# Performance work log

Hardware: AMD Instinct MI355X
Metric: run time of the kernel (lower is better)

The kernel has to match this reference:

```python
import jax, jax.numpy as jnp
import numpy as np

B, S, E = 4, 4096, 512
DK, DV = 64, 64


def setup_inputs() -> dict:
    key = jax.random.key(0)
    ks = jax.random.split(key, 7)
    s_e = 1.0 / np.sqrt(E)
    return {
        "embedding_matrix": jax.random.normal(ks[0], (B, S, E), dtype=jnp.float32),
        # torch Linear init ~ U(-1/sqrt(in), 1/sqrt(in)); stored here as [in, out]
        "Wq_w": jax.random.uniform(ks[1], (E, DK), jnp.float32, -s_e, s_e),
        "Wq_b": jax.random.uniform(ks[2], (DK,), jnp.float32, -s_e, s_e),
        "Wk_w": jax.random.uniform(ks[3], (E, DK), jnp.float32, -s_e, s_e),
        "Wk_b": jax.random.uniform(ks[4], (DK,), jnp.float32, -s_e, s_e),
        "Wv_w": jax.random.uniform(ks[5], (E, DV), jnp.float32, -s_e, s_e),
        "Wv_b": jax.random.uniform(ks[6], (DV,), jnp.float32, -s_e, s_e),
    }


def reference(embedding_matrix, Wq_w, Wq_b, Wk_w, Wk_b, Wv_w, Wv_b):
    # Single-head causal attention, faithful to the torch module (mask=True).
    Q = embedding_matrix @ Wq_w + Wq_b            # [B, S, DK]
    K = embedding_matrix @ Wk_w + Wk_b            # [B, S, DK]
    V = embedding_matrix @ Wv_w + Wv_b            # [B, S, DV]
    dk = K.shape[-1]
    scores = jnp.einsum('bqd,bkd->bqk', Q, K) / jnp.sqrt(jnp.asarray(dk, Q.dtype))
    seq_len = scores.shape[-1]
    causal = jnp.tril(jnp.ones((seq_len, seq_len), dtype=bool))  # keep lower-tri
    scores = jnp.where(causal[None, :, :], scores, -jnp.inf)
    attn = jax.nn.softmax(scores.astype(jnp.float32), axis=-1)
    return jnp.einsum('bqk,bkd->bqd', attn, V)
```

## Files before the change

kernel.cpp:

```cpp
#include <hip/hip_runtime.h>
#include <hip/hip_bf16.h>

#define B_ 4
#define S_ 4096
#define E_ 512
#define D_ 64

typedef float  f32x4  __attribute__((ext_vector_type(4)));
typedef float  f32x16 __attribute__((ext_vector_type(16)));
typedef short  s16x8  __attribute__((ext_vector_type(8)));

__device__ inline short f2bf(float f){
  unsigned u = __builtin_bit_cast(unsigned, f);
  u += 0x7fffu + ((u >> 16) & 1u);
  return (short)(u >> 16);
}
__device__ inline unsigned bfpack(float a, float b){
  unsigned ua = __builtin_bit_cast(unsigned, a);
  unsigned ub = __builtin_bit_cast(unsigned, b);
  ua += 0x7fffu + ((ua >> 16) & 1u);
  ub += 0x7fffu + ((ub >> 16) & 1u);
  return (ua >> 16) | (ub & 0xffff0000u);
}
__device__ inline float ex2(float x){ return __builtin_amdgcn_exp2f(x); }

#define QSCALE 0.18033688f


__global__ __launch_bounds__(256) void prep_kernel(const float* __restrict__ Wq,
                                                   const float* __restrict__ Wk,
                                                   const float* __restrict__ Wv,
                                                   short* __restrict__ Wtf){
  int o = blockIdx.x * 256 + threadIdx.x;
  int cbi = o >> 13;
  int l   = (o >> 3) & 63;
  int j   = o & 7;
  int kk  = (o >> 9) & 15;
  int n = cbi * 16 + (l & 15);
  int k = kk * 32 + (l >> 4) * 8 + j;
  const float* W = (n < 64) ? Wq : (n < 128 ? Wk : Wv);
  float v = W[k * 64 + (n & 63)];
  if (n < 64) v *= QSCALE;
  Wtf[o] = f2bf(v);
}

__global__ __launch_bounds__(256) void proj_kernel(const float* __restrict__ X,
                                                   const short* __restrict__ Wtf,
                                                   const float* __restrict__ bq,
                                                   const float* __restrict__ bk,
                                                   const float* __restrict__ bv,
                                                   short* __restrict__ Qf,
                                                   short* __restrict__ Kf,
                                                   short* __restrict__ Vf){
  __shared__ short Xs[1024 * 8];
  __shared__ short Os[16][136];
  __shared__ short OsT[64][24];

  const int tid = threadIdx.x;
  const int l = tid & 63, w = tid >> 6;
  const int c = l & 15,  g = l >> 4;
  const int r0 = blockIdx.x * 16;
  const int t  = (r0 >> 5) & 127;
  const int h  = (r0 >> 4) & 1;
  const int b  = r0 >> 12;

#pragma unroll
  for (int i = 0; i < 4; i++){
    int ch  = i * 256 + tid;
    int row = ch >> 6, gr = ch & 63;
    const float* xp = X + (size_t)(r0 + row) * E_ + gr * 8;
    f32x4 a0 = *reinterpret_cast<const f32x4*>(xp);
    f32x4 a1 = *reinterpret_cast<const f32x4*>(xp + 4);
    s16x8 hv;
#pragma unroll
    for (int q = 0; q < 4; q++){ hv[q] = f2bf(a0[q]); hv[4+q] = f2bf(a1[q]); }
    *reinterpret_cast<s16x8*>(&Xs[(row * 64 + (gr ^ (row & 7))) * 8]) = hv;
  }
  __syncthreads();

  f32x4 acc[3];
#pragma unroll
  for (int j = 0; j < 3; j++) acc[j] = (f32x4){0.f,0.f,0.f,0.f};

  for (int kk = 0; kk < 16; kk++){
    s16x8 af = *reinterpret_cast<const s16x8*>(&Xs[(c * 64 + ((kk * 4 + g) ^ (c & 7))) * 8]);
#pragma unroll
    for (int j = 0; j < 3; j++){
      int cbi = w * 3 + j;
      s16x8 bf = *reinterpret_cast<const s16x8*>(Wtf + (((size_t)(cbi * 16 + kk)) << 9) + (l << 3));
      acc[j] = __builtin_amdgcn_mfma_f32_16x16x32_bf16(af, bf, acc[j], 0, 0, 0);
    }
  }

#pragma unroll
  for (int j = 0; j < 3; j++){
    int cbi = w * 3 + j;
    int d = ((cbi & 3) << 4) + c;
    if (cbi < 8){
      float bias = (cbi < 4) ? bq[d] * QSCALE : bk[d];
      int col = (cbi < 4) ? d : (64 + d);
#pragma unroll
      for (int r = 0; r < 4; r++) Os[g * 4 + r][col] = f2bf(acc[j][r] + bias);
    } else {
      float bias = bv[d];
      union { unsigned long long u; short s[4]; } pk;
#pragma unroll
      for (int r = 0; r < 4; r++) pk.s[r] = f2bf(acc[j][r] + bias);
      *reinterpret_cast<unsigned long long*>(&OsT[d][g * 4]) = pk.u;
    }
  }
  __syncthreads();

  const size_t tbase = ((size_t)(b * 128 + t)) << 11;
  {
    int q = tid & 127;
    int N = q >> 5, hd = (q >> 4) & 1, lo16 = q & 15;
    int d0 = N * 16 + hd * 8;
    int col = (tid < 128) ? d0 : (64 + d0);
    s16x8 vv = *reinterpret_cast<const s16x8*>(&Os[lo16][col]);
    short* dst = (tid < 128 ? Qf : Kf) + tbase + N * 512 + hd * 256 + (h * 16 + lo16) * 8;
    *reinterpret_cast<s16x8*>(dst) = vv;
  }
  if (tid < 128){
    int hf = tid >> 6, ht = (tid >> 5) & 1, dl = tid & 31;
    s16x8 vv = *reinterpret_cast<const s16x8*>(&OsT[hf * 32 + dl][ht * 8]);
    short* dst = Vf + tbase + (h + 2 * hf) * 512 + ht * 256 + dl * 8;
    *reinterpret_cast<s16x8*>(dst) = vv;
  }
}

__global__ __launch_bounds__(512, 4) void attn_kernel(const short* __restrict__ Qf,
                                                      const short* __restrict__ Kf,
                                                      const short* __restrict__ Vf,
                                                      float* __restrict__ out){
  __shared__ float accw[8][32][64];
  __shared__ float mlw[8][32][2];
  __shared__ float corrw[8][32];

  const int tid = threadIdx.x;
  const int w  = tid >> 6;
  const int l  = tid & 63;
  const int lo = l & 31, hi = l >> 5;
  const int bid = blockIdx.x;
  const int b  = bid >> 7;
  const int t  = 127 - (bid & 127);
  const int q0 = t << 5;

  const short* qb = Qf + (((size_t)(b * 128 + t)) << 11) + (l << 3);
  s16x8 qf0 = *reinterpret_cast<const s16x8*>(qb);
  s16x8 qf1 = *reinterpret_cast<const s16x8*>(qb + 512);
  s16x8 qf2 = *reinterpret_cast<const s16x8*>(qb + 1024);
  s16x8 qf3 = *reinterpret_cast<const s16x8*>(qb + 1536);

  float m = -1e30f, ls = 0.f;
  f32x16 acc0, acc1;
#pragma unroll
  for (int r = 0; r < 16; r++){ acc0[r] = 0.f; acc1[r] = 0.f; }

  const int nkt = t + 1;
  for (int kt = w; kt < nkt; kt += 8){
    const int k0 = kt << 5;
    const short* kb = Kf + (((size_t)(b * 128 + kt)) << 11) + (l << 3);
    s16x8 kf0 = *reinterpret_cast<const s16x8*>(kb);
    s16x8 kf1 = *reinterpret_cast<const s16x8*>(kb + 512);
    s16x8 kf2 = *reinterpret_cast<const s16x8*>(kb + 1024);
    s16x8 kf3 = *reinterpret_cast<const s16x8*>(kb + 1536);
    const short* vb = Vf + (((size_t)(b * 128 + kt)) << 11) + (l << 3);
    s16x8 v00 = *reinterpret_cast<const s16x8*>(vb);
    s16x8 v01 = *reinterpret_cast<const s16x8*>(vb + 512);
    s16x8 v10 = *reinterpret_cast<const s16x8*>(vb + 1024);
    s16x8 v11 = *reinterpret_cast<const s16x8*>(vb + 1536);

    f32x16 s;
#pragma unroll
    for (int r = 0; r < 16; r++) s[r] = 0.f;
    s = __builtin_amdgcn_mfma_f32_32x32x16_bf16(kf0, qf0, s, 0, 0, 0);
    s = __builtin_amdgcn_mfma_f32_32x32x16_bf16(kf1, qf1, s, 0, 0, 0);
    s = __builtin_amdgcn_mfma_f32_32x32x16_bf16(kf2, qf2, s, 0, 0, 0);
    s = __builtin_amdgcn_mfma_f32_32x32x16_bf16(kf3, qf3, s, 0, 0, 0);

    if (k0 == q0){
#pragma unroll
      for (int r = 0; r < 16; r++){
        int key = (r & 3) + ((r >> 2) << 3) + (hi << 2);
        if (key > lo) s[r] = -1e30f;
      }
    }

    float x0 = fmaxf(s[0], s[1]),  x1 = fmaxf(s[2], s[3]);
    float x2 = fmaxf(s[4], s[5]),  x3 = fmaxf(s[6], s[7]);
    float x4 = fmaxf(s[8], s[9]),  x5 = fmaxf(s[10], s[11]);
    float x6 = fmaxf(s[12], s[13]), x7 = fmaxf(s[14], s[15]);
    float pm = fmaxf(fmaxf(fmaxf(x0, x1), fmaxf(x2, x3)),
                     fmaxf(fmaxf(x4, x5), fmaxf(x6, x7)));
    pm = fmaxf(pm, __shfl_xor(pm, 32));

    if (!__all(pm - m <= 8.0f)){
      float mn = fmaxf(m, pm);
      float corr = ex2(m - mn);
      if (hi == 0) corrw[w][lo] = corr;
      asm volatile("s_waitcnt lgkmcnt(0)" ::: "memory");
      __builtin_amdgcn_sched_barrier(0);
      f32x4 c0 = *reinterpret_cast<const f32x4*>(&corrw[w][(hi << 2)]);
      f32x4 c1 = *reinterpret_cast<const f32x4*>(&corrw[w][8 + (hi << 2)]);
      f32x4 c2 = *reinterpret_cast<const f32x4*>(&corrw[w][16 + (hi << 2)]);
      f32x4 c3 = *reinterpret_cast<const f32x4*>(&corrw[w][24 + (hi << 2)]);
#pragma unroll
      for (int r = 0; r < 4; r++){
        acc0[r]      *= c0[r]; acc1[r]      *= c0[r];
        acc0[4 + r]  *= c1[r]; acc1[4 + r]  *= c1[r];
        acc0[8 + r]  *= c2[r]; acc1[8 + r]  *= c2[r];
        acc0[12 + r] *= c3[r]; acc1[12 + r] *= c3[r];
      }
      ls *= corr;
      m = mn;
    }

#pragma unroll
    for (int r = 0; r < 16; r++) s[r] = ex2(s[r] - m);

    float y0 = s[0]+s[1], y1 = s[2]+s[3], y2 = s[4]+s[5], y3 = s[6]+s[7];
    float y4 = s[8]+s[9], y5 = s[10]+s[11], y6 = s[12]+s[13], y7 = s[14]+s[15];
    float rs = ((y0+y1)+(y2+y3)) + ((y4+y5)+(y6+y7));
    rs += __shfl_xor(rs, 32);
    ls += rs;

    unsigned pk0 = bfpack(s[0], s[1]),   pk1 = bfpack(s[2], s[3]);
    unsigned pk2 = bfpack(s[4], s[5]),   pk3 = bfpack(s[6], s[7]);
    unsigned pk4 = bfpack(s[8], s[9]),   pk5 = bfpack(s[10], s[11]);
    unsigned pk6 = bfpack(s[12], s[13]), pk7 = bfpack(s[14], s[15]);

    unsigned sd0 = hi ? pk0 : pk2, sd1 = hi ? pk1 : pk3;
    unsigned rv0 = (unsigned)__shfl_xor((int)sd0, 32);
    unsigned rv1 = (unsigned)__shfl_xor((int)sd1, 32);
    union { s16x8 v; unsigned u[4]; } A0, A1;
    A0.u[0] = hi ? rv0 : pk0; A0.u[1] = hi ? rv1 : pk1;
    A0.u[2] = hi ? pk2 : rv0; A0.u[3] = hi ? pk3 : rv1;

    unsigned sd2 = hi ? pk4 : pk6, sd3 = hi ? pk5 : pk7;
    unsigned rv2 = (unsigned)__shfl_xor((int)sd2, 32);
    unsigned rv3 = (unsigned)__shfl_xor((int)sd3, 32);
    A1.u[0] = hi ? rv2 : pk4; A1.u[1] = hi ? rv3 : pk5;
    A1.u[2] = hi ? pk6 : rv2; A1.u[3] = hi ? pk7 : rv3;

    acc0 = __builtin_amdgcn_mfma_f32_32x32x16_bf16(A0.v, v00, acc0, 0, 0, 0);
    acc0 = __builtin_amdgcn_mfma_f32_32x32x16_bf16(A1.v, v01, acc0, 0, 0, 0);
    acc1 = __builtin_amdgcn_mfma_f32_32x32x16_bf16(A0.v, v10, acc1, 0, 0, 0);
    acc1 = __builtin_amdgcn_mfma_f32_32x32x16_bf16(A1.v, v11, acc1, 0, 0, 0);
  }

#pragma unroll
  for (int r = 0; r < 16; r++){
    int q = (r & 3) + ((r >> 2) << 3) + (hi << 2);
    accw[w][q][lo]      = acc0[r];
    accw[w][q][32 + lo] = acc1[r];
  }
  if (hi == 0){ mlw[w][lo][0] = m; mlw[w][lo][1] = ls; }
  __syncthreads();

  {
    int q  = tid >> 4;
    int dg = (tid & 15) << 2;
    float M = mlw[0][q][0];
#pragma unroll
    for (int j = 1; j < 8; j++) M = fmaxf(M, mlw[j][q][0]);
    float L = 0.f;
    f32x4 o = (f32x4){0.f,0.f,0.f,0.f};
#pragma unroll
    for (int j = 0; j < 8; j++){
      float wt = ex2(mlw[j][q][0] - M);
      L += mlw[j][q][1] * wt;
      f32x4 a = *reinterpret_cast<const f32x4*>(&accw[j][q][dg]);
      o += a * wt;
    }
    f32x4 res = o * (1.f / L);
    *reinterpret_cast<f32x4*>(out + ((size_t)((b << 12) + q0 + q)) * D_ + dg) = res;
  }
}

extern "C" void kernel_launch(void* const* d_in, const int* in_sizes, int n_in,
                              void* d_out, int out_size, void* d_ws, size_t ws_size,
                              hipStream_t stream){
  const float* X  = (const float*)d_in[0];
  const float* Wq = (const float*)d_in[1];
  const float* bq = (const float*)d_in[2];
  const float* Wk = (const float*)d_in[3];
  const float* bk = (const float*)d_in[4];
  const float* Wv = (const float*)d_in[5];
  const float* bv = (const float*)d_in[6];
  float* out = (float*)d_out;

  char* base = (char*)d_ws;
  short* Wtf = (short*)(base);
  short* Qf  = (short*)(base + 196608);
  short* Kf  = (short*)(base + 196608 + 2097152);
  short* Vf  = (short*)(base + 196608 + 2 * 2097152);

  prep_kernel<<<384, 256, 0, stream>>>(Wq, Wk, Wv, Wtf);
  proj_kernel<<<1024, 256, 0, stream>>>(X, Wtf, bq, bk, bv, Qf, Kf, Vf);
  attn_kernel<<<512, 512, 0, stream>>>(Qf, Kf, Vf, out);
}
```

Measured before the change: 120.7 us.

## Prefetch next K/V tile in registers and interleave causal block order across batches

Software-pipelines the attention loop so each wave loads the next K/V tile into registers while the current tile's MFMAs and softmax run, hiding global-load latency. It also remaps block IDs so the first two batches schedule long causal tiles first and the last two schedule short tiles first, mixing heavy and light blocks across the dispatch order. The cost is extra VGPRs for the double-buffered fragments, which could hurt occupancy at 512 threads with 4 blocks per CU, plus a redundant reload on the last iteration.

```diff
diff --git a/kernel.cpp b/kernel.cpp
--- a/kernel.cpp
+++ b/kernel.cpp
@@ -142,8 +142,10 @@
   const int l  = tid & 63;
   const int lo = l & 31, hi = l >> 5;
   const int bid = blockIdx.x;
-  const int b  = bid >> 7;
-  const int t  = 127 - (bid & 127);
+  const int jj = bid & 255, kk2 = bid >> 8;
+  const int b  = (kk2 << 1) | (jj >> 7);
+  const int t0 = jj & 127;
+  const int t  = kk2 ? t0 : 127 - t0;
   const int q0 = t << 5;
 
   const short* qb = Qf + (((size_t)(b * 128 + t)) << 11) + (l << 3);
@@ -158,26 +160,44 @@
   for (int r = 0; r < 16; r++){ acc0[r] = 0.f; acc1[r] = 0.f; }
 
   const int nkt = t + 1;
-  for (int kt = w; kt < nkt; kt += 8){
+  const size_t kvb = ((size_t)(b * 128)) << 11;
+
+  int kt = w;
+  s16x8 ck0, ck1, ck2, ck3, cv0, cv1, cv2, cv3;
+  if (kt < nkt){
+    const short* kb = Kf + kvb + (((size_t)kt) << 11) + (l << 3);
+    ck0 = *reinterpret_cast<const s16x8*>(kb);
+    ck1 = *reinterpret_cast<const s16x8*>(kb + 512);
+    ck2 = *reinterpret_cast<const s16x8*>(kb + 1024);
+    ck3 = *reinterpret_cast<const s16x8*>(kb + 1536);
+    const short* vb = Vf + kvb + (((size_t)kt) << 11) + (l << 3);
+    cv0 = *reinterpret_cast<const s16x8*>(vb);
+    cv1 = *reinterpret_cast<const s16x8*>(vb + 512);
+    cv2 = *reinterpret_cast<const s16x8*>(vb + 1024);
+    cv3 = *reinterpret_cast<const s16x8*>(vb + 1536);
+  }
+
+  for (; kt < nkt; kt += 8){
     const int k0 = kt << 5;
-    const short* kb = Kf + (((size_t)(b * 128 + kt)) << 11) + (l << 3);
-    s16x8 kf0 = *reinterpret_cast<const s16x8*>(kb);
-    s16x8 kf1 = *reinterpret_cast<const s16x8*>(kb + 512);
-    s16x8 kf2 = *reinterpret_cast<const s16x8*>(kb + 1024);
-    s16x8 kf3 = *reinterpret_cast<const s16x8*>(kb + 1536);
-    const short* vb = Vf + (((size_t)(b * 128 + kt)) << 11) + (l << 3);
-    s16x8 v00 = *reinterpret_cast<const s16x8*>(vb);
-    s16x8 v01 = *reinterpret_cast<const s16x8*>(vb + 512);
-    s16x8 v10 = *reinterpret_cast<const s16x8*>(vb + 1024);
-    s16x8 v11 = *reinterpret_cast<const s16x8*>(vb + 1536);
+    const int ktn = (kt + 8 < nkt) ? (kt + 8) : kt;
+    const short* kbn = Kf + kvb + (((size_t)ktn) << 11) + (l << 3);
+    s16x8 nk0 = *reinterpret_cast<const s16x8*>(kbn);
+    s16x8 nk1 = *reinterpret_cast<const s16x8*>(kbn + 512);
+    s16x8 nk2 = *reinterpret_cast<const s16x8*>(kbn + 1024);
+    s16x8 nk3 = *reinterpret_cast<const s16x8*>(kbn + 1536);
+    const short* vbn = Vf + kvb + (((size_t)ktn) << 11) + (l << 3);
+    s16x8 nv0 = *reinterpret_cast<const s16x8*>(vbn);
+    s16x8 nv1 = *reinterpret_cast<const s16x8*>(vbn + 512);
+    s16x8 nv2 = *reinterpret_cast<const s16x8*>(vbn + 1024);
+    s16x8 nv3 = *reinterpret_cast<const s16x8*>(vbn + 1536);
 
     f32x16 s;
 #pragma unroll
     for (int r = 0; r < 16; r++) s[r] = 0.f;
-    s = __builtin_amdgcn_mfma_f32_32x32x16_bf16(kf0, qf0, s, 0, 0, 0);
-    s = __builtin_amdgcn_mfma_f32_32x32x16_bf16(kf1, qf1, s, 0, 0, 0);
-    s = __builtin_amdgcn_mfma_f32_32x32x16_bf16(kf2, qf2, s, 0, 0, 0);
-    s = __builtin_amdgcn_mfma_f32_32x32x16_bf16(kf3, qf3, s, 0, 0, 0);
+    s = __builtin_amdgcn_mfma_f32_32x32x16_bf16(ck0, qf0, s, 0, 0, 0);
+    s = __builtin_amdgcn_mfma_f32_32x32x16_bf16(ck1, qf1, s, 0, 0, 0);
+    s = __builtin_amdgcn_mfma_f32_32x32x16_bf16(ck2, qf2, s, 0, 0, 0);
+    s = __builtin_amdgcn_mfma_f32_32x32x16_bf16(ck3, qf3, s, 0, 0, 0);
 
     if (k0 == q0){
 #pragma unroll
@@ -243,10 +263,13 @@
     A1.u[0] = hi ? rv2 : pk4; A1.u[1] = hi ? rv3 : pk5;
     A1.u[2] = hi ? pk6 : rv2; A1.u[3] = hi ? pk7 : rv3;
 
-    acc0 = __builtin_amdgcn_mfma_f32_32x32x16_bf16(A0.v, v00, acc0, 0, 0, 0);
-    acc0 = __builtin_amdgcn_mfma_f32_32x32x16_bf16(A1.v, v01, acc0, 0, 0, 0);
-    acc1 = __builtin_amdgcn_mfma_f32_32x32x16_bf16(A0.v, v10, acc1, 0, 0, 0);
-    acc1 = __builtin_amdgcn_mfma_f32_32x32x16_bf16(A1.v, v11, acc1, 0, 0, 0);
+    acc0 = __builtin_amdgcn_mfma_f32_32x32x16_bf16(A0.v, cv0, acc0, 0, 0, 0);
+    acc0 = __builtin_amdgcn_mfma_f32_32x32x16_bf16(A1.v, cv1, acc0, 0, 0, 0);
+    acc1 = __builtin_amdgcn_mfma_f32_32x32x16_bf16(A0.v, cv2, acc1, 0, 0, 0);
+    acc1 = __builtin_amdgcn_mfma_f32_32x32x16_bf16(A1.v, cv3, acc1, 0, 0, 0);
+
+    ck0 = nk0; ck1 = nk1; ck2 = nk2; ck3 = nk3;
+    cv0 = nv0; cv1 = nv1; cv2 = nv2; cv3 = nv3;
   }
 
 #pragma unroll
```

New measurement: 132.0 us. +9.4%, slower.
